# Optimization experiments

Measured on AMD Instinct MI355X. Metric: run time of the kernel, lower is better.

## Reference

```python
import jax, jax.numpy as jnp
import numpy as np

N, E, C, S = 30000, 480000, 256, 4
T_EVO = 0.1        # evolution_time
MAX_EIG = 0.5      # max_eigenval in create_ultra_stable_hamiltonian
MAX_NORM = 0.01    # max_norm in ultra_stable_matrix_exp
MAX_TERMS = 4
LN_EPS = 1e-5


def _build_subgraphs(edge_index, n, s):
    """Emulates the per-node k_hop=1 BFS (capped at max_subgraph_size=s) and the
    subgraph laplacian Hamiltonian build (edge_weight=0.1, self-loops added).
    Pure structural preprocessing: integer/constant w.r.t. all float params."""
    src = np.asarray(edge_index[0], dtype=np.int64)
    dst = np.asarray(edge_index[1], dtype=np.int64)
    loops = np.arange(n, dtype=np.int64)
    src = np.concatenate([src, loops]); dst = np.concatenate([dst, loops])
    order = np.argsort(src, kind='stable')
    src_s, dst_s = src[order], dst[order]
    starts = np.searchsorted(src_s, np.arange(n))
    ends = np.searchsorted(src_s, np.arange(n) + 1)
    edge_set = set((src * n + dst).tolist())
    sub_nodes = np.zeros((n, s), dtype=np.int64)
    sub_mask = np.zeros((n, s), dtype=np.float32)
    H = np.zeros((n, s, s), dtype=np.float32)
    for i in range(n):
        nbrs = [i]
        for d in dst_s[starts[i]:ends[i]]:
            d = int(d)
            if d != i and d not in nbrs:
                nbrs.append(d)
                if len(nbrs) == s:
                    break
        m = len(nbrs)
        sub_nodes[i, :m] = nbrs
        sub_nodes[i, m:] = i          # pad with center (masked out below)
        sub_mask[i, :m] = 1.0
        A = np.zeros((s, s), dtype=np.float32)
        for a in range(m):
            ka = nbrs[a] * n
            for b in range(m):
                if (ka + nbrs[b]) in edge_set:
                    A[a, b] = 1.0
        deg = np.maximum(A.sum(axis=1), 1e-6)   # degree(row), clamped like torch
        H[i] = np.diag(deg) - 0.1 * A           # laplacian with edge_weight=0.1
    return sub_nodes, sub_mask, H


def _mat_fro(M):
    return jnp.sqrt(jnp.sum(jnp.abs(M) ** 2, axis=(-2, -1)))


def _unitary_from_H(sub_H):
    """ultra_stable_matrix_exp, batched over N tiny [S,S] Hamiltonians.
    The torch .item() norm/eigenvalue rescales detach gradients, so treating this
    whole block as parameter-independent (it is: H is structural) is faithful."""
    Hc = sub_H.astype(jnp.complex64)
    ev = jnp.linalg.eigvals(Hc)                              # [N,S] (CPU op)
    mx = jnp.max(ev.real, axis=-1)
    Hc = Hc * jnp.where(mx > MAX_EIG, MAX_EIG / mx, 1.0)[:, None, None]
    hn = _mat_fro(Hc)
    Hc = Hc * jnp.where(hn > MAX_NORM, MAX_NORM / hn, 1.0)[:, None, None]
    A = (-1j) * Hc * (T_EVO * 0.1)                           # scaled_H
    I = jnp.eye(S, dtype=jnp.complex64)
    U = jnp.broadcast_to(I, Hc.shape)
    term = U
    for k in range(1, MAX_TERMS + 1):
        term = jnp.matmul(term, A) / k
        tn = _mat_fro(term)
        term = term * jnp.where(tn > 0.1, 0.1 / tn, 1.0)[:, None, None]
        U = U + term
    err = _mat_fro(jnp.matmul(U, jnp.conj(jnp.swapaxes(U, -1, -2))) - I)
    U = jnp.where((err > 0.1)[:, None, None], I + A * 0.01, U)
    return U


def _cplx_linear(xr, xi, wr, wi, br, bi):
    xr = jnp.clip(xr, -10.0, 10.0); xi = jnp.clip(xi, -10.0, 10.0)
    re = xr @ wr.T - xi @ wi.T + br
    im = xr @ wi.T + xi @ wr.T + bi
    return re + 1j * im


def _cln(z, w, b, eps=LN_EPS):
    # UltraStableComplexLayerNorm, training-mode batch stats over dim 0
    mag = jnp.clip(jnp.sqrt(z.real ** 2 + z.imag ** 2 + eps), eps, 1000.0)
    mean = mag.mean(0)
    var = mag.var(0)
    nm = (mag - mean) / (jnp.sqrt(var + eps) + eps)
    sm = jnp.clip(nm * jnp.abs(w) + b, eps, 10.0)
    ph = jnp.arctan2(jnp.clip(z.imag, -1e6, 1e6), jnp.clip(z.real, -1e6, 1e6) + 1e-10)
    return sm * jnp.cos(ph) + 1j * (sm * jnp.sin(ph))


def _crelu(z, leak=0.01, mx=5.0):
    r = jnp.clip(z.real, -mx, mx); i = jnp.clip(z.imag, -mx, mx)
    return jnp.where(r > 0, r, leak * r) + 1j * jnp.where(i > 0, i, leak * i)


def setup_inputs() -> dict:
    key = jax.random.key(0)
    k1, k2, k3, k4 = jax.random.split(key, 4)
    x = jax.random.normal(k1, (N, C), dtype=jnp.float32)
    edge_index = jax.random.randint(k2, (2, E), 0, N, dtype=jnp.int64)
    sub_nodes, sub_mask, sub_H = _build_subgraphs(np.asarray(edge_index), N, S)
    std = np.sqrt(0.5 / C).astype(np.float32)
    w_real = jax.random.normal(k3, (C, C), dtype=jnp.float32) * std
    w_imag = jax.random.normal(k4, (C, C), dtype=jnp.float32) * std
    return {
        'x': x,
        'edge_index': edge_index,
        'sub_nodes': jnp.asarray(sub_nodes),
        'sub_mask': jnp.asarray(sub_mask),
        'sub_H': jnp.asarray(sub_H),
        'w_real': w_real,
        'w_imag': w_imag,
        'b_real': jnp.zeros((C,), jnp.float32),
        'b_imag': jnp.zeros((C,), jnp.float32),
        'ln_weight': jnp.full((C,), 0.1, jnp.float32),
        'ln_bias': jnp.zeros((C,), jnp.float32),
        'evolution_scale': jnp.asarray(0.1, jnp.float32),
    }


def reference(x, edge_index, sub_nodes, sub_mask, sub_H,
              w_real, w_imag, b_real, b_imag, ln_weight, ln_bias,
              evolution_scale):
    # complex linear (input is real -> imag part zero, matching torch.complex(x, 0*x))
    h = _cplx_linear(x, jnp.zeros_like(x), w_real, w_imag, b_real, b_imag)  # [N,C] c64
    U = _unitary_from_H(sub_H)                                              # [N,S,S]
    sub_x = h[sub_nodes] * sub_mask[..., None]                              # [N,S,C]
    # center node is slot 0 of each subgraph -> take row 0 of U @ sub_x
    evolved = jnp.einsum('ns,nsc->nc', U[:, 0, :], sub_x)
    out = evolved * evolution_scale + x.astype(jnp.complex64)  # residual (in==out)
    out = _cln(out, ln_weight, ln_bias)
    out = _crelu(out)
    # dropout is eval-mode identity
    return jnp.concatenate([out.real, out.imag], axis=-1)      # [N, 2C] float32
```

## Files before the change

kernel.cpp:

```cpp
#include <hip/hip_runtime.h>
#include <stdint.h>

#define N_NODES 30000
#define NC 256

typedef _Float16 f16x8 __attribute__((ext_vector_type(8)));
typedef _Float16 f16x4 __attribute__((ext_vector_type(4)));
typedef _Float16 f16x2 __attribute__((ext_vector_type(2)));
typedef float f32x4 __attribute__((ext_vector_type(4)));

__global__ void k_conv_x(const float* __restrict__ x, _Float16* __restrict__ xb) {
    int i = (blockIdx.x * 256 + threadIdx.x) * 4;
    float4 v = *reinterpret_cast<const float4*>(x + i);
    f16x4 o;
    o[0] = (_Float16)fminf(fmaxf(v.x, -10.f), 10.f);
    o[1] = (_Float16)fminf(fmaxf(v.y, -10.f), 10.f);
    o[2] = (_Float16)fminf(fmaxf(v.z, -10.f), 10.f);
    o[3] = (_Float16)fminf(fmaxf(v.w, -10.f), 10.f);
    *reinterpret_cast<f16x4*>(xb + i) = o;
}

__global__ void k_conv_w(const float* __restrict__ wr, const float* __restrict__ wi,
                         _Float16* __restrict__ Wb) {
    int i = (blockIdx.x * 256 + threadIdx.x) * 4;
    const float* src = (i < NC * NC) ? (wr + i) : (wi + (i - NC * NC));
    float4 v = *reinterpret_cast<const float4*>(src);
    f16x4 o;
    o[0] = (_Float16)v.x; o[1] = (_Float16)v.y;
    o[2] = (_Float16)v.z; o[3] = (_Float16)v.w;
    *reinterpret_cast<f16x4*>(Wb + i) = o;
}

__global__ __launch_bounds__(256, 2) void k_gemm(
    const _Float16* __restrict__ A, const _Float16* __restrict__ B,
    const float* __restrict__ br, const float* __restrict__ bi,
    _Float16* __restrict__ H)
{
    int bid = blockIdx.x;
    int bm = bid >> 1, cs = bid & 1;
    int tid = threadIdx.x;
    int lane = tid & 63, wave = tid >> 6;
    int quad = lane >> 4, l16 = lane & 15;
    int wm = wave >> 1, wn = wave & 1;
    int row0 = bm * 128 + wm * 64;

    f16x8 af[4][8];
#pragma unroll
    for (int mi = 0; mi < 4; mi++) {
        int r = row0 + mi * 16 + l16;
        if (r >= N_NODES) r = N_NODES - 1;
        const _Float16* ap = A + r * NC + quad * 8;
#pragma unroll
        for (int kc = 0; kc < 8; kc++)
            af[mi][kc] = *reinterpret_cast<const f16x8*>(ap + kc * 32);
    }

    const float* bias_p = wn ? bi : br;
#pragma unroll
    for (int cn = 0; cn < 2; cn++) {
        const _Float16* bbase = B + ((wn ? 256 : 0) + cs * 128 + cn * 64 + l16) * NC
                                  + quad * 8;
        f16x8 bb[2][4];
#pragma unroll
        for (int ni = 0; ni < 4; ni++)
            bb[0][ni] = *reinterpret_cast<const f16x8*>(bbase + ni * 16 * NC);
        f32x4 acc[4][4] = {};
#pragma unroll
        for (int kc = 0; kc < 8; kc++) {
            int cur = kc & 1, nxt = cur ^ 1;
            if (kc < 7) {
#pragma unroll
                for (int ni = 0; ni < 4; ni++)
                    bb[nxt][ni] = *reinterpret_cast<const f16x8*>(
                        bbase + ni * 16 * NC + (kc + 1) * 32);
            }
#pragma unroll
            for (int mi = 0; mi < 4; mi++)
#pragma unroll
                for (int ni = 0; ni < 4; ni++)
                    acc[mi][ni] = __builtin_amdgcn_mfma_f32_16x16x32_f16(
                        af[mi][kc], bb[cur][ni], acc[mi][ni], 0, 0, 0);
        }
#pragma unroll
        for (int ni = 0; ni < 4; ni++) {
            int c = cs * 128 + cn * 64 + ni * 16 + l16;
            float bias = bias_p[c];
            int cc = 2 * c + wn;
#pragma unroll
            for (int mi = 0; mi < 4; mi++) {
                int rowb = row0 + mi * 16 + quad * 4;
#pragma unroll
                for (int r = 0; r < 4; r++) {
                    int row = rowb + r;
                    if (row < N_NODES)
                        H[row * 512 + cc] = (_Float16)(acc[mi][ni][r] + bias);
                }
            }
        }
    }
}

#define NPB 30
__global__ __launch_bounds__(256) void k_evolve(
    const float* __restrict__ x, const int* __restrict__ sub_nodes,
    const float* __restrict__ sub_mask, const float* __restrict__ subH,
    const _Float16* __restrict__ h, const float* __restrict__ escp,
    float* __restrict__ outz, _Float16* __restrict__ zbuf, int use_f16,
    float* __restrict__ ssum, float* __restrict__ ssumsq)
{
    __shared__ int   s_nodes[NPB][4];
    __shared__ float s_g[NPB][4];
    __shared__ float s_m0[NPB];
    __shared__ float s_redA[4][256];
    __shared__ float s_redB[4][256];
    int tid = threadIdx.x;
    int g = tid >> 6, lane = tid & 63;
    int base = blockIdx.x * NPB;
    if (tid < NPB) {
        int node = base + tid;
        float fr = 0.f;
#pragma unroll
        for (int t = 0; t < 16; t++) { float v = subH[node * 16 + t]; fr += v * v; }
        float coef = 1e-4f * rsqrtf(fr);
#pragma unroll
        for (int s = 0; s < 4; s++) {
            s_g[tid][s]     = coef * subH[node * 16 + s] * sub_mask[node * 4 + s];
            s_nodes[tid][s] = sub_nodes[node * 4 + s];
        }
        s_m0[tid] = sub_mask[node * 4];
    }
    __syncthreads();
    float esc = *escp;
    float lsum[4] = {0.f, 0.f, 0.f, 0.f};
    float lsq[4]  = {0.f, 0.f, 0.f, 0.f};
    for (int j = g; j < NPB; j += 4) {
        int node = base + j;
        f16x8 hv[4];
#pragma unroll
        for (int s = 0; s < 4; s++)
            hv[s] = *reinterpret_cast<const f16x8*>(h + s_nodes[j][s] * 512 + lane * 8);
        float4 x4 = *reinterpret_cast<const float4*>(x + node * NC + lane * 4);
        float xr[4] = {x4.x, x4.y, x4.z, x4.w};
        float G[4] = {s_g[j][0], s_g[j][1], s_g[j][2], s_g[j][3]};
        float m0 = s_m0[j];
        f16x8 zo;
        float or4[4], oi4[4];
#pragma unroll
        for (int e = 0; e < 4; e++) {
            float hr0 = (float)hv[0][2 * e], hi0 = (float)hv[0][2 * e + 1];
            float er = m0 * hr0, ei = m0 * hi0;
#pragma unroll
            for (int s = 0; s < 4; s++) {
                float hr = (float)hv[s][2 * e], hi = (float)hv[s][2 * e + 1];
                er = fmaf(G[s], hi, er);
                ei = fmaf(-G[s], hr, ei);
            }
            float outr = fmaf(esc, er, xr[e]);
            float outi = esc * ei;
            or4[e] = outr; oi4[e] = outi;
            zo[2 * e] = (_Float16)outr; zo[2 * e + 1] = (_Float16)outi;
            float mag = sqrtf(fmaf(outr, outr, fmaf(outi, outi, 1e-5f)));
            mag = fminf(fmaxf(mag, 1e-5f), 1000.f);
            lsum[e] += mag;
            lsq[e] = fmaf(mag, mag, lsq[e]);
        }
        if (use_f16) {
            *reinterpret_cast<f16x8*>(zbuf + node * 512 + lane * 8) = zo;
        } else {
            *reinterpret_cast<float4*>(outz + node * 512 + lane * 4) =
                make_float4(or4[0], or4[1], or4[2], or4[3]);
            *reinterpret_cast<float4*>(outz + node * 512 + 256 + lane * 4) =
                make_float4(oi4[0], oi4[1], oi4[2], oi4[3]);
        }
    }
#pragma unroll
    for (int e = 0; e < 4; e++) {
        s_redA[g][lane * 4 + e] = lsum[e];
        s_redB[g][lane * 4 + e] = lsq[e];
    }
    __syncthreads();
    float a = s_redA[0][tid] + s_redA[1][tid] + s_redA[2][tid] + s_redA[3][tid];
    float b = s_redB[0][tid] + s_redB[1][tid] + s_redB[2][tid] + s_redB[3][tid];
    atomicAdd(&ssum[tid], a);
    atomicAdd(&ssumsq[tid], b);
}

__global__ __launch_bounds__(256) void k_norm(
    float* __restrict__ out, const _Float16* __restrict__ zbuf, int use_f16,
    const float* __restrict__ ssum, const float* __restrict__ ssumsq,
    const float* __restrict__ lnw, const float* __restrict__ lnb)
{
    int tid = threadIdx.x;
    int node = blockIdx.x * 4 + (tid >> 6);
    int c0 = (tid & 63) * 4;
    float re[4], im[4];
    if (use_f16) {
        f16x8 z = *reinterpret_cast<const f16x8*>(zbuf + node * 512 + c0 * 2);
#pragma unroll
        for (int e = 0; e < 4; e++) { re[e] = (float)z[2 * e]; im[e] = (float)z[2 * e + 1]; }
    } else {
        float4 r4 = *reinterpret_cast<const float4*>(out + node * 512 + c0);
        float4 i4 = *reinterpret_cast<const float4*>(out + node * 512 + 256 + c0);
        re[0] = r4.x; re[1] = r4.y; re[2] = r4.z; re[3] = r4.w;
        im[0] = i4.x; im[1] = i4.y; im[2] = i4.z; im[3] = i4.w;
    }
    float4 s4 = *reinterpret_cast<const float4*>(ssum + c0);
    float4 q4 = *reinterpret_cast<const float4*>(ssumsq + c0);
    float4 w4 = *reinterpret_cast<const float4*>(lnw + c0);
    float4 lb4 = *reinterpret_cast<const float4*>(lnb + c0);
    float S[4] = {s4.x, s4.y, s4.z, s4.w};
    float Q[4] = {q4.x, q4.y, q4.z, q4.w};
    float W[4] = {w4.x, w4.y, w4.z, w4.w};
    float L[4] = {lb4.x, lb4.y, lb4.z, lb4.w};
    const float invN = 1.0f / (float)N_NODES;
    float orr[4], oii[4];
#pragma unroll
    for (int e = 0; e < 4; e++) {
        float mean = S[e] * invN;
        float var = fmaxf(Q[e] * invN - mean * mean, 0.f);
        float denom = sqrtf(var + 1e-5f) + 1e-5f;
        float A = fabsf(W[e]) / denom;
        float Bc = L[e] - mean * A;
        float r = re[e], i = im[e];
        float mag = sqrtf(fmaf(r, r, fmaf(i, i, 1e-5f)));
        mag = fminf(fmaxf(mag, 1e-5f), 1000.f);
        float sm = fmaf(mag, A, Bc);
        sm = fminf(fmaxf(sm, 1e-5f), 10.0f);
        float px = fminf(fmaxf(r, -1e6f), 1e6f) + 1e-10f;
        float py = fminf(fmaxf(i, -1e6f), 1e6f);
        float r2 = fmaf(px, px, py * py);
        float inv = rsqrtf(r2);
        float zr = sm * px * inv, zi = sm * py * inv;
        zr = fminf(fmaxf(zr, -5.f), 5.f);
        zi = fminf(fmaxf(zi, -5.f), 5.f);
        orr[e] = zr > 0.f ? zr : 0.01f * zr;
        oii[e] = zi > 0.f ? zi : 0.01f * zi;
    }
    *reinterpret_cast<float4*>(out + node * 512 + c0) =
        make_float4(orr[0], orr[1], orr[2], orr[3]);
    *reinterpret_cast<float4*>(out + node * 512 + 256 + c0) =
        make_float4(oii[0], oii[1], oii[2], oii[3]);
}

extern "C" void kernel_launch(void* const* d_in, const int* in_sizes, int n_in,
                              void* d_out, int out_size, void* d_ws, size_t ws_size,
                              hipStream_t stream) {
    const float* x        = (const float*)d_in[0];
    const int*   sub_nodes = (const int*)d_in[2];
    const float* sub_mask  = (const float*)d_in[3];
    const float* subH      = (const float*)d_in[4];
    const float* wr  = (const float*)d_in[5];
    const float* wi  = (const float*)d_in[6];
    const float* br  = (const float*)d_in[7];
    const float* bi  = (const float*)d_in[8];
    const float* lnw = (const float*)d_in[9];
    const float* lnb = (const float*)d_in[10];
    const float* esc = (const float*)d_in[11];
    float* out = (float*)d_out;

    char* ws = (char*)d_ws;
    const size_t XB_OFF   = 0;
    const size_t WB_OFF   = 15360000;
    const size_t H_OFF    = 15622144;
    const size_t STAT_OFF = 46342144;
    const size_t ZB_OFF   = 46346240;
    const size_t WS_NEED_F16 = ZB_OFF + 30720000;
    _Float16* xb = (_Float16*)(ws + XB_OFF);
    _Float16* Wb = (_Float16*)(ws + WB_OFF);
    _Float16* h  = (_Float16*)(ws + H_OFF);
    float* ssum   = (float*)(ws + STAT_OFF);
    float* ssumsq = (float*)(ws + STAT_OFF + 1024);
    _Float16* zbuf = (_Float16*)(ws + ZB_OFF);
    int use_f16 = (ws_size >= WS_NEED_F16) ? 1 : 0;

    hipMemsetAsync(ssum, 0, 2048, stream);
    hipLaunchKernelGGL(k_conv_x, dim3(7500), dim3(256), 0, stream, x, xb);
    hipLaunchKernelGGL(k_conv_w, dim3(128), dim3(256), 0, stream, wr, wi, Wb);
    hipLaunchKernelGGL(k_gemm, dim3(235 * 2), dim3(256), 0, stream, xb, Wb, br, bi, h);
    hipLaunchKernelGGL(k_evolve, dim3(1000), dim3(256), 0, stream,
                       x, sub_nodes, sub_mask, subH, h, esc, out, zbuf, use_f16,
                       ssum, ssumsq);
    hipLaunchKernelGGL(k_norm, dim3(7500), dim3(256), 0, stream,
                       out, zbuf, use_f16, ssum, ssumsq, lnw, lnb);
}
```

Before: 211.8 us.

## Precompute per-node evolution coefficients and double-buffer gathers in evolve kernel

Adds a small prep kernel that folds the Frobenius-norm coefficient, mask and evolution scale into four per-node coefficients, so evolve no longer recomputes them from subH. The evolve kernel moves to 512-thread blocks with 60 nodes each and software-pipelines the neighbour-row gathers, prefetching the next node's h rows and x while computing the current one. The aggregated-stat reduction is split across two thread halves, which halves the number of atomics per node. The cost is an extra kernel launch, a small extra workspace buffer, and more registers per thread for the prefetch buffers.

```diff
diff --git a/kernel.cpp b/kernel.cpp
--- a/kernel.cpp
+++ b/kernel.cpp
@@ -29,6 +29,27 @@
     o[0] = (_Float16)v.x; o[1] = (_Float16)v.y;
     o[2] = (_Float16)v.z; o[3] = (_Float16)v.w;
     *reinterpret_cast<f16x4*>(Wb + i) = o;
+}
+
+__global__ void k_prep(const float* __restrict__ subH, const float* __restrict__ sub_mask,
+                       const float* __restrict__ escp, float* __restrict__ c4) {
+    int node = blockIdx.x * 256 + threadIdx.x;
+    if (node >= N_NODES) return;
+    float esc = *escp;
+    const float4* Hp = reinterpret_cast<const float4*>(subH + node * 16);
+    float4 r0 = Hp[0], r1 = Hp[1], r2 = Hp[2], r3 = Hp[3];
+    float fr = r0.x * r0.x + r0.y * r0.y + r0.z * r0.z + r0.w * r0.w
+             + r1.x * r1.x + r1.y * r1.y + r1.z * r1.z + r1.w * r1.w
+             + r2.x * r2.x + r2.y * r2.y + r2.z * r2.z + r2.w * r2.w
+             + r3.x * r3.x + r3.y * r3.y + r3.z * r3.z + r3.w * r3.w;
+    float coef = 1e-4f * rsqrtf(fr) * esc;
+    float4 m = *reinterpret_cast<const float4*>(sub_mask + node * 4);
+    float4 o;
+    o.x = coef * r0.x * m.x;
+    o.y = coef * r0.y * m.y;
+    o.z = coef * r0.z * m.z;
+    o.w = coef * r0.w * m.w;
+    *reinterpret_cast<float4*>(c4 + node * 4) = o;
 }
 
 __global__ __launch_bounds__(256, 2) void k_gemm(
@@ -100,78 +121,95 @@
     }
 }
 
-#define NPB 30
-__global__ __launch_bounds__(256) void k_evolve(
+#define NPB 60
+#define NGRP 8
+__global__ __launch_bounds__(512) void k_evolve(
     const float* __restrict__ x, const int* __restrict__ sub_nodes,
-    const float* __restrict__ sub_mask, const float* __restrict__ subH,
-    const _Float16* __restrict__ h, const float* __restrict__ escp,
+    const float* __restrict__ c4, const _Float16* __restrict__ h,
+    const float* __restrict__ escp,
     float* __restrict__ outz, _Float16* __restrict__ zbuf, int use_f16,
     float* __restrict__ ssum, float* __restrict__ ssumsq)
 {
     __shared__ int   s_nodes[NPB][4];
-    __shared__ float s_g[NPB][4];
-    __shared__ float s_m0[NPB];
-    __shared__ float s_redA[4][256];
-    __shared__ float s_redB[4][256];
+    __shared__ float s_P[NPB][4];
+    __shared__ float s_redA[NGRP][256];
+    __shared__ float s_redB[NGRP][256];
     int tid = threadIdx.x;
     int g = tid >> 6, lane = tid & 63;
     int base = blockIdx.x * NPB;
     if (tid < NPB) {
         int node = base + tid;
-        float fr = 0.f;
-#pragma unroll
-        for (int t = 0; t < 16; t++) { float v = subH[node * 16 + t]; fr += v * v; }
-        float coef = 1e-4f * rsqrtf(fr);
-#pragma unroll
-        for (int s = 0; s < 4; s++) {
-            s_g[tid][s]     = coef * subH[node * 16 + s] * sub_mask[node * 4 + s];
-            s_nodes[tid][s] = sub_nodes[node * 4 + s];
-        }
-        s_m0[tid] = sub_mask[node * 4];
+        *reinterpret_cast<float4*>(&s_P[tid][0]) =
+            *reinterpret_cast<const float4*>(c4 + node * 4);
+        *reinterpret_cast<int4*>(&s_nodes[tid][0]) =
+            *reinterpret_cast<const int4*>(sub_nodes + node * 4);
     }
     __syncthreads();
     float esc = *escp;
     float lsum[4] = {0.f, 0.f, 0.f, 0.f};
     float lsq[4]  = {0.f, 0.f, 0.f, 0.f};
-    for (int j = g; j < NPB; j += 4) {
-        int node = base + j;
-        f16x8 hv[4];
-#pragma unroll
-        for (int s = 0; s < 4; s++)
-            hv[s] = *reinterpret_cast<const f16x8*>(h + s_nodes[j][s] * 512 + lane * 8);
-        float4 x4 = *reinterpret_cast<const float4*>(x + node * NC + lane * 4);
-        float xr[4] = {x4.x, x4.y, x4.z, x4.w};
-        float G[4] = {s_g[j][0], s_g[j][1], s_g[j][2], s_g[j][3]};
-        float m0 = s_m0[j];
-        f16x8 zo;
-        float or4[4], oi4[4];
-#pragma unroll
-        for (int e = 0; e < 4; e++) {
-            float hr0 = (float)hv[0][2 * e], hi0 = (float)hv[0][2 * e + 1];
-            float er = m0 * hr0, ei = m0 * hi0;
-#pragma unroll
-            for (int s = 0; s < 4; s++) {
-                float hr = (float)hv[s][2 * e], hi = (float)hv[s][2 * e + 1];
-                er = fmaf(G[s], hi, er);
-                ei = fmaf(-G[s], hr, ei);
+
+    f16x8 hvA[4];
+    float4 xA;
+    int j = g;
+#pragma unroll
+    for (int s = 0; s < 4; s++)
+        hvA[s] = *reinterpret_cast<const f16x8*>(h + s_nodes[j][s] * 512 + lane * 8);
+    xA = *reinterpret_cast<const float4*>(x + (base + j) * NC + lane * 4);
+
+    for (;;) {
+        int jn = j + NGRP;
+        bool more = jn < NPB;
+        f16x8 hvB[4];
+        float4 xB;
+        if (more) {
+#pragma unroll
+            for (int s = 0; s < 4; s++)
+                hvB[s] = *reinterpret_cast<const f16x8*>(
+                    h + s_nodes[jn][s] * 512 + lane * 8);
+            xB = *reinterpret_cast<const float4*>(x + (base + jn) * NC + lane * 4);
+        }
+        {
+            int node = base + j;
+            float P0 = s_P[j][0], P1 = s_P[j][1], P2 = s_P[j][2], P3 = s_P[j][3];
+            float xr[4] = {xA.x, xA.y, xA.z, xA.w};
+            f16x8 zo;
+            float or4[4], oi4[4];
+#pragma unroll
+            for (int e = 0; e < 4; e++) {
+                float hr0 = (float)hvA[0][2 * e], hi0 = (float)hvA[0][2 * e + 1];
+                float hr1 = (float)hvA[1][2 * e], hi1 = (float)hvA[1][2 * e + 1];
+                float hr2 = (float)hvA[2][2 * e], hi2 = (float)hvA[2][2 * e + 1];
+                float hr3 = (float)hvA[3][2 * e], hi3 = (float)hvA[3][2 * e + 1];
+                float er = esc * hr0;
+                float ei = esc * hi0;
+                er = fmaf(P0, hi0, er); ei = fmaf(-P0, hr0, ei);
+                er = fmaf(P1, hi1, er); ei = fmaf(-P1, hr1, ei);
+                er = fmaf(P2, hi2, er); ei = fmaf(-P2, hr2, ei);
+                er = fmaf(P3, hi3, er); ei = fmaf(-P3, hr3, ei);
+                float outr = er + xr[e];
+                float outi = ei;
+                or4[e] = outr; oi4[e] = outi;
+                zo[2 * e] = (_Float16)outr; zo[2 * e + 1] = (_Float16)outi;
+                float mag = sqrtf(fmaf(outr, outr, fmaf(outi, outi, 1e-5f)));
+                mag = fminf(fmaxf(mag, 1e-5f), 1000.f);
+                lsum[e] += mag;
+                lsq[e] = fmaf(mag, mag, lsq[e]);
             }
-            float outr = fmaf(esc, er, xr[e]);
-            float outi = esc * ei;
-            or4[e] = outr; oi4[e] = outi;
-            zo[2 * e] = (_Float16)outr; zo[2 * e + 1] = (_Float16)outi;
-            float mag = sqrtf(fmaf(outr, outr, fmaf(outi, outi, 1e-5f)));
-            mag = fminf(fmaxf(mag, 1e-5f), 1000.f);
-            lsum[e] += mag;
-            lsq[e] = fmaf(mag, mag, lsq[e]);
+            if (use_f16) {
+                *reinterpret_cast<f16x8*>(zbuf + node * 512 + lane * 8) = zo;
+            } else {
+                *reinterpret_cast<float4*>(outz + node * 512 + lane * 4) =
+                    make_float4(or4[0], or4[1], or4[2], or4[3]);
+                *reinterpret_cast<float4*>(outz + node * 512 + 256 + lane * 4) =
+                    make_float4(oi4[0], oi4[1], oi4[2], oi4[3]);
+            }
         }
-        if (use_f16) {
-            *reinterpret_cast<f16x8*>(zbuf + node * 512 + lane * 8) = zo;
-        } else {
-            *reinterpret_cast<float4*>(outz + node * 512 + lane * 4) =
-                make_float4(or4[0], or4[1], or4[2], or4[3]);
-            *reinterpret_cast<float4*>(outz + node * 512 + 256 + lane * 4) =
-                make_float4(oi4[0], oi4[1], oi4[2], oi4[3]);
-        }
+        if (!more) break;
+#pragma unroll
+        for (int s = 0; s < 4; s++) hvA[s] = hvB[s];
+        xA = xB;
+        j = jn;
     }
 #pragma unroll
     for (int e = 0; e < 4; e++) {
@@ -179,10 +217,18 @@
         s_redB[g][lane * 4 + e] = lsq[e];
     }
     __syncthreads();
-    float a = s_redA[0][tid] + s_redA[1][tid] + s_redA[2][tid] + s_redA[3][tid];
-    float b = s_redB[0][tid] + s_redB[1][tid] + s_redB[2][tid] + s_redB[3][tid];
-    atomicAdd(&ssum[tid], a);
-    atomicAdd(&ssumsq[tid], b);
+    if (tid < 256) {
+        float a = 0.f;
+#pragma unroll
+        for (int q = 0; q < NGRP; q++) a += s_redA[q][tid];
+        atomicAdd(&ssum[tid], a);
+    } else {
+        int t = tid - 256;
+        float b = 0.f;
+#pragma unroll
+        for (int q = 0; q < NGRP; q++) b += s_redB[q][t];
+        atomicAdd(&ssumsq[t], b);
+    }
 }
 
 __global__ __launch_bounds__(256) void k_norm(
@@ -263,22 +309,26 @@
     const size_t WB_OFF   = 15360000;
     const size_t H_OFF    = 15622144;
     const size_t STAT_OFF = 46342144;
-    const size_t ZB_OFF   = 46346240;
+    const size_t C4_OFF   = 46346240;
+    const size_t ZB_OFF   = 46826240;
     const size_t WS_NEED_F16 = ZB_OFF + 30720000;
     _Float16* xb = (_Float16*)(ws + XB_OFF);
     _Float16* Wb = (_Float16*)(ws + WB_OFF);
     _Float16* h  = (_Float16*)(ws + H_OFF);
     float* ssum   = (float*)(ws + STAT_OFF);
     float* ssumsq = (float*)(ws + STAT_OFF + 1024);
+    float* c4     = (float*)(ws + C4_OFF);
     _Float16* zbuf = (_Float16*)(ws + ZB_OFF);
     int use_f16 = (ws_size >= WS_NEED_F16) ? 1 : 0;
 
     hipMemsetAsync(ssum, 0, 2048, stream);
     hipLaunchKernelGGL(k_conv_x, dim3(7500), dim3(256), 0, stream, x, xb);
     hipLaunchKernelGGL(k_conv_w, dim3(128), dim3(256), 0, stream, wr, wi, Wb);
+    hipLaunchKernelGGL(k_prep, dim3(118), dim3(256), 0, stream,
+                       subH, sub_mask, esc, c4);
     hipLaunchKernelGGL(k_gemm, dim3(235 * 2), dim3(256), 0, stream, xb, Wb, br, bi, h);
-    hipLaunchKernelGGL(k_evolve, dim3(1000), dim3(256), 0, stream,
-                       x, sub_nodes, sub_mask, subH, h, esc, out, zbuf, use_f16,
+    hipLaunchKernelGGL(k_evolve, dim3(500), dim3(512), 0, stream,
+                       x, sub_nodes, c4, h, esc, out, zbuf, use_f16,
                        ssum, ssumsq);
     hipLaunchKernelGGL(k_norm, dim3(7500), dim3(256), 0, stream,
                        out, zbuf, use_f16, ssum, ssumsq, lnw, lnb);
```

Result: faster. 200.1 us (-5.5%).
